# Optimization experiments

Measured on AMD Instinct MI355X. Metric: run time of the kernel, lower is better.

The kernel has to match this reference:

```python
import jax, jax.numpy as jnp
import numpy as np

N, IN_DIM, H, L, NH, LAT = 4096, 16, 128, 4, 8, 16
HD = H // NH
FF = 2 * H
DR_THR = 0.2
LN_EPS = 1e-5


def _ln(x, s, b):
    m = x.mean(-1, keepdims=True)
    v = ((x - m) ** 2).mean(-1, keepdims=True)
    return (x - m) * jax.lax.rsqrt(v + LN_EPS) * s + b


def compute_dr_mask(x_raw):
    eta = x_raw[:, 1] * (2.62 - (-2.62)) + (-2.62)
    phi = x_raw[:, 2] * (3.1416 - (-3.1416)) + (-3.1416)
    deta = eta[:, None] - eta[None, :]
    dphi = phi[:, None] - phi[None, :]
    dphi = jnp.arctan2(jnp.sin(dphi), jnp.cos(dphi))
    dr = jnp.sqrt(deta ** 2 + dphi ** 2)
    return jnp.where(dr <= DR_THR, 0.0, -jnp.inf).astype(jnp.float32)


def setup_inputs() -> dict:
    key = jax.random.key(0)
    ks = jax.random.split(key, 32)
    g = lambda i, shape, s=0.02: (jax.random.normal(ks[i], shape, dtype=jnp.float32) * s)
    inp = {
        'x_raw': jax.random.uniform(ks[0], (N, IN_DIM), dtype=jnp.float32),
        'batch': jnp.zeros((N,), dtype=jnp.int64) if jax.config.read('jax_enable_x64') else jnp.zeros((N,), dtype=jnp.int32),
        'in_w': g(1, (H, IN_DIM), 0.1), 'in_b': jnp.zeros((H,), jnp.float32),
        'ln1_s': jnp.ones((L, H), jnp.float32), 'ln1_b': jnp.zeros((L, H), jnp.float32),
        'qkv_w': g(2, (L, 3 * H, H)), 'qkv_b': jnp.zeros((L, 3 * H), jnp.float32),
        'ao_w': g(3, (L, H, H)), 'ao_b': jnp.zeros((L, H), jnp.float32),
        'ln2_s': jnp.ones((L, H), jnp.float32), 'ln2_b': jnp.zeros((L, H), jnp.float32),
        'f1_w': g(4, (L, FF, H)), 'f1_b': jnp.zeros((L, FF), jnp.float32),
        'f2_w': g(5, (L, H, FF)), 'f2_b': jnp.zeros((L, H), jnp.float32),
        'lat1_w': g(6, (H, H), 0.08), 'lat1_b': jnp.zeros((H,), jnp.float32),
        'lat2_w': g(7, (LAT, H), 0.08), 'lat2_b': jnp.zeros((LAT,), jnp.float32),
        'b1_w': g(8, (H // 2, H), 0.08), 'b1_b': jnp.zeros((H // 2,), jnp.float32),
        'b2_w': g(9, (1, H // 2), 0.008), 'b2_b': jnp.full((1,), -3.0, jnp.float32),
    }
    return inp


def reference(x_raw, batch, in_w, in_b, ln1_s, ln1_b, qkv_w, qkv_b, ao_w, ao_b,
              ln2_s, ln2_b, f1_w, f1_b, f2_w, f2_b,
              lat1_w, lat1_b, lat2_w, lat2_b, b1_w, b1_b, b2_w, b2_b):
    mask = jax.lax.stop_gradient(compute_dr_mask(x_raw))  # [N, N] additive mask
    x = x_raw @ in_w.T + in_b  # [N, H]
    scale = 1.0 / jnp.sqrt(jnp.float32(HD))
    for l in range(L):  # norm_first TransformerEncoderLayer, eval mode (no dropout)
        h = _ln(x, ln1_s[l], ln1_b[l])
        qkv = h @ qkv_w[l].T + qkv_b[l]
        q, k, v = [t.reshape(N, NH, HD) for t in jnp.split(qkv, 3, axis=-1)]
        scores = jnp.einsum('qhd,khd->hqk', q, k) * scale + mask[None]
        attn = jax.nn.softmax(scores, axis=-1)
        o = jnp.einsum('hqk,khd->qhd', attn, v).reshape(N, H)
        x = x + o @ ao_w[l].T + ao_b[l]
        h2 = _ln(x, ln2_s[l], ln2_b[l])
        x = x + jax.nn.relu(h2 @ f1_w[l].T + f1_b[l]) @ f2_w[l].T + f2_b[l]
    lat = jax.nn.relu(x @ lat1_w.T + lat1_b) @ lat2_w.T + lat2_b  # [N, LAT]
    lat = lat / jnp.maximum(jnp.linalg.norm(lat, axis=-1, keepdims=True), 1e-12)
    beta = jax.nn.sigmoid(jax.nn.relu(x @ b1_w.T + b1_b) @ b2_w.T + b2_b)
    beta = jnp.clip(beta, 1e-6, 1 - 1e-6)  # [N, 1]
    return beta, lat
```

## Files before the change

kernel.cpp:

```cpp
#include <hip/hip_runtime.h>
#include <hip/hip_bf16.h>

typedef unsigned short u16;
typedef short short8_t __attribute__((ext_vector_type(8)));
typedef float floatx4 __attribute__((ext_vector_type(4)));

constexpr int NT = 4096, H = 128, CAP = 64;
constexpr int GRID = 256, BLK = 512, GSTRIDE = GRID * BLK;

constexpr int OFF_QKV  = 0;
constexpr int OFF_AO   = 196608;
constexpr int OFF_F1   = 262144;
constexpr int OFF_F2   = 393216;
constexpr int OFF_LAT1 = 524288;
constexpr int OFF_B1   = 540672;
constexpr int OFF_LAT2 = 548864;
constexpr int W_TOTAL  = 550912;

__device__ __forceinline__ float bfu(u16 u) { return __uint_as_float(((unsigned)u) << 16); }
__device__ __forceinline__ u16 f2bf(float f) {
  unsigned u = __float_as_uint(f);
  u += 0x7fffu + ((u >> 16) & 1u);
  return (u16)(u >> 16);
}
__device__ __forceinline__ void unpack8(uint4 u, float* f) {
  f[0] = __uint_as_float(u.x << 16); f[1] = __uint_as_float(u.x & 0xffff0000u);
  f[2] = __uint_as_float(u.y << 16); f[3] = __uint_as_float(u.y & 0xffff0000u);
  f[4] = __uint_as_float(u.z << 16); f[5] = __uint_as_float(u.z & 0xffff0000u);
  f[6] = __uint_as_float(u.w << 16); f[7] = __uint_as_float(u.w & 0xffff0000u);
}
__device__ __forceinline__ short8_t cvt8(const float* bp) {
  const float4 f0 = *(const float4*)bp, f1 = *(const float4*)(bp + 4);
  short8_t r;
  r[0] = (short)f2bf(f0.x); r[1] = (short)f2bf(f0.y);
  r[2] = (short)f2bf(f0.z); r[3] = (short)f2bf(f0.w);
  r[4] = (short)f2bf(f1.x); r[5] = (short)f2bf(f1.y);
  r[6] = (short)f2bf(f1.z); r[7] = (short)f2bf(f1.w);
  return r;
}

struct Prm {
  const float *xr, *in_w, *in_b, *ln1_s, *ln1_b, *qkv_w, *qkv_b, *ao_w, *ao_b,
              *ln2_s, *ln2_b, *f1_w, *f1_b, *f2_w, *f2_b, *lat1_w, *lat1_b,
              *lat2_w, *lat2_b, *b1_w, *b1_b, *b2_w, *b2_b;
  u16* W; u16* QKV0; u16* QKV1; float* Xg; int* NI; int* NC; float* out;
};

__global__ __launch_bounds__(BLK, 2) void prep_kernel(Prm p) {
  const int t = threadIdx.x, bid = blockIdx.x;
  const int lane = t & 63, w = t >> 6;
  const int lr = lane & 15, quad = lane >> 4;
  const int gtid = bid * BLK + t;
  const int r0 = bid * 16;
  const floatx4 FZ = {0.f, 0.f, 0.f, 0.f};

  __shared__ float Xs[16][132];
  __shared__ union {
    unsigned long long words[8][64];
    struct { u16 A16[16][152]; } g;
    u16 QS[16][384];
  } sm;

  for (int i = 49152 + gtid; i < W_TOTAL; i += GSTRIDE) {
    float v;
    if      (i < OFF_AO)   v = p.qkv_w[i];
    else if (i < OFF_F1)   v = p.ao_w[i - OFF_AO];
    else if (i < OFF_F2)   v = p.f1_w[i - OFF_F1];
    else if (i < OFF_LAT1) v = p.f2_w[i - OFF_F2];
    else if (i < OFF_B1)   v = p.lat1_w[i - OFF_LAT1];
    else if (i < OFF_LAT2) v = p.b1_w[i - OFF_B1];
    else                   v = p.lat2_w[i - OFF_LAT2];
    p.W[i] = f2bf(v);
  }
  for (int i = t; i < 16 * H; i += BLK) {
    const int r = i >> 7, c = i & 127;
    const float* xp = p.xr + (size_t)(r0 + r) * 16;
    const float* wp = p.in_w + c * 16;
    float acc = p.in_b[c];
#pragma unroll
    for (int k = 0; k < 16; ++k) acc += xp[k] * wp[k];
    Xs[r][c] = acc;
    p.Xg[(size_t)(r0 + r) * H + c] = acc;
  }
  for (int uu = 0; uu < 2; ++uu) {
    const int q0 = r0 + uu * 8;
    double qe[8], qp_[8];
#pragma unroll
    for (int j = 0; j < 8; ++j) {
      qe[j]  = (double)p.xr[(q0 + j) * 16 + 1] * 5.24 - 2.62;
      qp_[j] = (double)p.xr[(q0 + j) * 16 + 2] * 6.2832 - 3.1416;
    }
    for (int c = 0; c < 8; ++c) {
      const int k = c * 512 + t;
      const double ke = (double)p.xr[k * 16 + 1] * 5.24 - 2.62;
      const double kp = (double)p.xr[k * 16 + 2] * 6.2832 - 3.1416;
#pragma unroll
      for (int j = 0; j < 8; ++j) {
        const double de = qe[j] - ke;
        double dp = qp_[j] - kp;
        dp -= 6.283185307179586 * rint(dp * 0.15915494309189535);
        const unsigned long long bm = __ballot((de * de + dp * dp) <= 0.04);
        if (lane == 0) sm.words[j][c * 8 + w] = bm;
      }
    }
    __syncthreads();
    {
      unsigned long long m = sm.words[w][lane];
      const int cnt = __popcll(m);
      int incl = cnt;
#pragma unroll
      for (int off = 1; off < 64; off <<= 1) {
        const int n = __shfl_up(incl, off);
        if (lane >= off) incl += n;
      }
      int pos = incl - cnt;
      const int qq = q0 + w;
      const int kbase = (lane >> 3) * 512 + (lane & 7) * 64;
      while (m) {
        const int b = __builtin_ctzll(m);
        m &= m - 1;
        if (pos < CAP) p.NI[qq * CAP + pos] = kbase + b;
        ++pos;
      }
      if (lane == 63) p.NC[qq] = incl > CAP ? CAP : incl;
    }
    __syncthreads();
  }
  {
    const int r = t >> 5, j0 = (t & 31) * 4;
    const float4 xv = *(const float4*)&Xs[r][j0];
    float v0 = xv.x, v1 = xv.y, v2 = xv.z, v3 = xv.w;
    float s = v0 + v1 + v2 + v3;
    float ss = v0 * v0 + v1 * v1 + v2 * v2 + v3 * v3;
#pragma unroll
    for (int off = 1; off <= 16; off <<= 1) {
      s += __shfl_xor(s, off); ss += __shfl_xor(ss, off);
    }
    const float mean = s * (1.f / 128.f);
    const float rstd = rsqrtf(ss * (1.f / 128.f) - mean * mean + 1e-5f);
    v0 = (v0 - mean) * rstd * p.ln1_s[j0]     + p.ln1_b[j0];
    v1 = (v1 - mean) * rstd * p.ln1_s[j0 + 1] + p.ln1_b[j0 + 1];
    v2 = (v2 - mean) * rstd * p.ln1_s[j0 + 2] + p.ln1_b[j0 + 2];
    v3 = (v3 - mean) * rstd * p.ln1_s[j0 + 3] + p.ln1_b[j0 + 3];
    uint2 pk;
    pk.x = (unsigned)f2bf(v0) | ((unsigned)f2bf(v1) << 16);
    pk.y = (unsigned)f2bf(v2) | ((unsigned)f2bf(v3) << 16);
    *(uint2*)&sm.g.A16[r][j0] = pk;
  }
  __syncthreads();
  {
    const int c0 = w * 48;
    floatx4 a0 = FZ, a1 = FZ, a2 = FZ;
#pragma unroll
    for (int k0 = 0; k0 < 128; k0 += 32) {
      short8_t a  = *(const short8_t*)&sm.g.A16[lr][k0 + quad * 8];
      short8_t b0 = cvt8(&p.qkv_w[(size_t)(c0 + lr) * 128 + k0 + quad * 8]);
      short8_t b1 = cvt8(&p.qkv_w[(size_t)(c0 + 16 + lr) * 128 + k0 + quad * 8]);
      short8_t b2 = cvt8(&p.qkv_w[(size_t)(c0 + 32 + lr) * 128 + k0 + quad * 8]);
      a0 = __builtin_amdgcn_mfma_f32_16x16x32_bf16(a, b0, a0, 0, 0, 0);
      a1 = __builtin_amdgcn_mfma_f32_16x16x32_bf16(a, b1, a1, 0, 0, 0);
      a2 = __builtin_amdgcn_mfma_f32_16x16x32_bf16(a, b2, a2, 0, 0, 0);
    }
    __syncthreads();
#pragma unroll
    for (int r = 0; r < 4; ++r) {
      const int row = quad * 4 + r;
      sm.QS[row][c0 + lr]      = f2bf(a0[r] + p.qkv_b[c0 + lr]);
      sm.QS[row][c0 + 16 + lr] = f2bf(a1[r] + p.qkv_b[c0 + 16 + lr]);
      sm.QS[row][c0 + 32 + lr] = f2bf(a2[r] + p.qkv_b[c0 + 32 + lr]);
    }
    __syncthreads();
    unsigned long long* d64 = (unsigned long long*)(p.QKV0 + (size_t)r0 * 384);
    const unsigned long long* s64 = (const unsigned long long*)&sm.QS[0][0];
    for (int j = t; j < 1536; j += BLK) d64[j] = s64[j];
  }
}

__global__ __launch_bounds__(BLK, 2) void layer_kernel(Prm p, int l,
                                                       const u16* __restrict__ qsrc,
                                                       u16* __restrict__ qdst) {
  const int t = threadIdx.x, bid = blockIdx.x;
  const int lane = t & 63, w = t >> 6;
  const int lr = lane & 15, quad = lane >> 4;
  const int r0 = bid * 16;
  const floatx4 FZ = {0.f, 0.f, 0.f, 0.f};

  __shared__ float Xs[16][132];
  __shared__ int NIs[16][CAP];
  __shared__ int NCs[16];
  __shared__ union {
    struct { u16 A16[16][152]; u16 FF1[16][280]; } g;
    u16 QS[16][384];
  } sm;

  {
    const int r = t >> 5, j0 = (t & 31) * 4;
    *(float4*)&Xs[r][j0] = *(const float4*)&p.Xg[(size_t)(r0 + r) * H + j0];
    for (int j = t; j < 16 * CAP; j += BLK) (&NIs[0][0])[j] = p.NI[r0 * CAP + j];
    if (t < 16) NCs[t] = p.NC[r0 + t];
  }

  auto stage_x = [&](const float* sc, const float* bi, bool do_ln) {
    const int r = t >> 5, j0 = (t & 31) * 4;
    const float4 xv = *(const float4*)&Xs[r][j0];
    float v0 = xv.x, v1 = xv.y, v2 = xv.z, v3 = xv.w;
    if (do_ln) {
      float s = v0 + v1 + v2 + v3;
      float ss = v0 * v0 + v1 * v1 + v2 * v2 + v3 * v3;
#pragma unroll
      for (int off = 1; off <= 16; off <<= 1) {
        s += __shfl_xor(s, off); ss += __shfl_xor(ss, off);
      }
      const float mean = s * (1.f / 128.f);
      const float rstd = rsqrtf(ss * (1.f / 128.f) - mean * mean + 1e-5f);
      v0 = (v0 - mean) * rstd * sc[j0]     + bi[j0];
      v1 = (v1 - mean) * rstd * sc[j0 + 1] + bi[j0 + 1];
      v2 = (v2 - mean) * rstd * sc[j0 + 2] + bi[j0 + 2];
      v3 = (v3 - mean) * rstd * sc[j0 + 3] + bi[j0 + 3];
    }
    uint2 pk;
    pk.x = (unsigned)f2bf(v0) | ((unsigned)f2bf(v1) << 16);
    pk.y = (unsigned)f2bf(v2) | ((unsigned)f2bf(v3) << 16);
    *(uint2*)&sm.g.A16[r][j0] = pk;
  };
  __syncthreads();

  {
    const int pr = t >> 2, sub = t & 3;
    const int lq = pr >> 3, h = pr & 7;
    const u16* qp = qsrc + (size_t)(r0 + lq) * 384 + h * 16;
    float qv[16];
    { uint4 a = *(const uint4*)qp, b = *(const uint4*)(qp + 8);
      unpack8(a, qv); unpack8(b, qv + 8); }
#pragma unroll
    for (int d = 0; d < 16; ++d) qv[d] *= 0.25f;
    float o[16];
#pragma unroll
    for (int d = 0; d < 16; ++d) o[d] = 0.f;
    float se = 0.f;
    const int cnt = NCs[lq];
    for (int i = sub; i < cnt; i += 4) {
      const int nb = NIs[lq][i];
      const u16* kp = qsrc + (size_t)nb * 384 + 128 + h * 16;
      float kv[16], vv[16];
      { uint4 a = *(const uint4*)kp;         uint4 b = *(const uint4*)(kp + 8);
        unpack8(a, kv); unpack8(b, kv + 8); }
      { uint4 a = *(const uint4*)(kp + 128); uint4 b = *(const uint4*)(kp + 136);
        unpack8(a, vv); unpack8(b, vv + 8); }
      float s0 = 0.f, s1 = 0.f, s2 = 0.f, s3 = 0.f;
#pragma unroll
      for (int d = 0; d < 16; d += 4) {
        s0 += qv[d] * kv[d];         s1 += qv[d + 1] * kv[d + 1];
        s2 += qv[d + 2] * kv[d + 2]; s3 += qv[d + 3] * kv[d + 3];
      }
      const float e = expf((s0 + s1) + (s2 + s3));
      se += e;
#pragma unroll
      for (int d = 0; d < 16; ++d) o[d] += e * vv[d];
    }
#pragma unroll
    for (int d = 0; d < 16; ++d) o[d] += __shfl_xor(o[d], 1);
    se += __shfl_xor(se, 1);
#pragma unroll
    for (int d = 0; d < 16; ++d) o[d] += __shfl_xor(o[d], 2);
    se += __shfl_xor(se, 2);
    if (sub == 0) {
      const float inv = 1.f / se;
      uint4 w0, w1;
      w0.x = (unsigned)f2bf(o[0] * inv)  | ((unsigned)f2bf(o[1] * inv) << 16);
      w0.y = (unsigned)f2bf(o[2] * inv)  | ((unsigned)f2bf(o[3] * inv) << 16);
      w0.z = (unsigned)f2bf(o[4] * inv)  | ((unsigned)f2bf(o[5] * inv) << 16);
      w0.w = (unsigned)f2bf(o[6] * inv)  | ((unsigned)f2bf(o[7] * inv) << 16);
      w1.x = (unsigned)f2bf(o[8] * inv)  | ((unsigned)f2bf(o[9] * inv) << 16);
      w1.y = (unsigned)f2bf(o[10] * inv) | ((unsigned)f2bf(o[11] * inv) << 16);
      w1.z = (unsigned)f2bf(o[12] * inv) | ((unsigned)f2bf(o[13] * inv) << 16);
      w1.w = (unsigned)f2bf(o[14] * inv) | ((unsigned)f2bf(o[15] * inv) << 16);
      *(uint4*)&sm.g.A16[lq][h * 16]     = w0;
      *(uint4*)&sm.g.A16[lq][h * 16 + 8] = w1;
    }
  }
  __syncthreads();
  {
    const u16* Bw = p.W + OFF_AO + l * 16384;
    const float* ab = p.ao_b + l * 128;
    const int col = w * 16 + lr;
    floatx4 acc = FZ;
#pragma unroll
    for (int k0 = 0; k0 < 128; k0 += 32) {
      short8_t a = *(const short8_t*)&sm.g.A16[lr][k0 + quad * 8];
      short8_t b = *(const short8_t*)&Bw[(size_t)col * 128 + k0 + quad * 8];
      acc = __builtin_amdgcn_mfma_f32_16x16x32_bf16(a, b, acc, 0, 0, 0);
    }
    const float bv = ab[col];
#pragma unroll
    for (int r = 0; r < 4; ++r)
      Xs[quad * 4 + r][col] += acc[r] + bv;
  }
  __syncthreads();
  stage_x(p.ln2_s + l * 128, p.ln2_b + l * 128, true);
  __syncthreads();
  {
    const u16* Bw = p.W + OFF_F1 + l * 32768;
    const float* fb = p.f1_b + l * 256;
    const int c0 = w * 32;
    floatx4 a0 = FZ, a1 = FZ;
#pragma unroll
    for (int k0 = 0; k0 < 128; k0 += 32) {
      short8_t a  = *(const short8_t*)&sm.g.A16[lr][k0 + quad * 8];
      short8_t b0 = *(const short8_t*)&Bw[(size_t)(c0 + lr) * 128 + k0 + quad * 8];
      short8_t b1 = *(const short8_t*)&Bw[(size_t)(c0 + 16 + lr) * 128 + k0 + quad * 8];
      a0 = __builtin_amdgcn_mfma_f32_16x16x32_bf16(a, b0, a0, 0, 0, 0);
      a1 = __builtin_amdgcn_mfma_f32_16x16x32_bf16(a, b1, a1, 0, 0, 0);
    }
#pragma unroll
    for (int r = 0; r < 4; ++r) {
      const int row = quad * 4 + r;
      sm.g.FF1[row][c0 + lr]      = f2bf(fmaxf(a0[r] + fb[c0 + lr], 0.f));
      sm.g.FF1[row][c0 + 16 + lr] = f2bf(fmaxf(a1[r] + fb[c0 + 16 + lr], 0.f));
    }
  }
  __syncthreads();
  {
    const u16* Bw = p.W + OFF_F2 + l * 32768;
    const float* fb = p.f2_b + l * 128;
    const int col = w * 16 + lr;
    floatx4 acc = FZ;
#pragma unroll
    for (int k0 = 0; k0 < 256; k0 += 32) {
      short8_t a = *(const short8_t*)&sm.g.FF1[lr][k0 + quad * 8];
      short8_t b = *(const short8_t*)&Bw[(size_t)col * 256 + k0 + quad * 8];
      acc = __builtin_amdgcn_mfma_f32_16x16x32_bf16(a, b, acc, 0, 0, 0);
    }
    const float bv = fb[col];
#pragma unroll
    for (int r = 0; r < 4; ++r)
      Xs[quad * 4 + r][col] += acc[r] + bv;
  }
  __syncthreads();
  if (l < 3) {
    {
      const int r = t >> 5, j0 = (t & 31) * 4;
      *(float4*)&p.Xg[(size_t)(r0 + r) * H + j0] = *(const float4*)&Xs[r][j0];
    }
    stage_x(p.ln1_s + (l + 1) * 128, p.ln1_b + (l + 1) * 128, true);
    __syncthreads();
    {
      const u16* Bw = p.W + OFF_QKV + (l + 1) * 49152;
      const float* qb = p.qkv_b + (l + 1) * 384;
      const int c0 = w * 48;
      floatx4 a0 = FZ, a1 = FZ, a2 = FZ;
#pragma unroll
      for (int k0 = 0; k0 < 128; k0 += 32) {
        short8_t a  = *(const short8_t*)&sm.g.A16[lr][k0 + quad * 8];
        short8_t b0 = *(const short8_t*)&Bw[(size_t)(c0 + lr) * 128 + k0 + quad * 8];
        short8_t b1 = *(const short8_t*)&Bw[(size_t)(c0 + 16 + lr) * 128 + k0 + quad * 8];
        short8_t b2 = *(const short8_t*)&Bw[(size_t)(c0 + 32 + lr) * 128 + k0 + quad * 8];
        a0 = __builtin_amdgcn_mfma_f32_16x16x32_bf16(a, b0, a0, 0, 0, 0);
        a1 = __builtin_amdgcn_mfma_f32_16x16x32_bf16(a, b1, a1, 0, 0, 0);
        a2 = __builtin_amdgcn_mfma_f32_16x16x32_bf16(a, b2, a2, 0, 0, 0);
      }
      __syncthreads();
#pragma unroll
      for (int r = 0; r < 4; ++r) {
        const int row = quad * 4 + r;
        sm.QS[row][c0 + lr]      = f2bf(a0[r] + qb[c0 + lr]);
        sm.QS[row][c0 + 16 + lr] = f2bf(a1[r] + qb[c0 + 16 + lr]);
        sm.QS[row][c0 + 32 + lr] = f2bf(a2[r] + qb[c0 + 32 + lr]);
      }
      __syncthreads();
      unsigned long long* d64 = (unsigned long long*)(qdst + (size_t)r0 * 384);
      const unsigned long long* s64 = (const unsigned long long*)&sm.QS[0][0];
      for (int j = t; j < 1536; j += BLK) d64[j] = s64[j];
    }
  } else {
    stage_x(nullptr, nullptr, false);
    __syncthreads();
    {
      const int c0 = w * 32;
      if (c0 < 192) {
        const u16* Bw = p.W + OFF_LAT1;
        floatx4 a0 = FZ, a1 = FZ;
#pragma unroll
        for (int k0 = 0; k0 < 128; k0 += 32) {
          short8_t a  = *(const short8_t*)&sm.g.A16[lr][k0 + quad * 8];
          short8_t b0 = *(const short8_t*)&Bw[(size_t)(c0 + lr) * 128 + k0 + quad * 8];
          short8_t b1 = *(const short8_t*)&Bw[(size_t)(c0 + 16 + lr) * 128 + k0 + quad * 8];
          a0 = __builtin_amdgcn_mfma_f32_16x16x32_bf16(a, b0, a0, 0, 0, 0);
          a1 = __builtin_amdgcn_mfma_f32_16x16x32_bf16(a, b1, a1, 0, 0, 0);
        }
        const int cA = c0 + lr, cB = c0 + 16 + lr;
        const float bA = cA < 128 ? p.lat1_b[cA] : p.b1_b[cA - 128];
        const float bB = cB < 128 ? p.lat1_b[cB] : p.b1_b[cB - 128];
#pragma unroll
        for (int r = 0; r < 4; ++r) {
          const int row = quad * 4 + r;
          sm.g.FF1[row][cA] = f2bf(fmaxf(a0[r] + bA, 0.f));
          sm.g.FF1[row][cB] = f2bf(fmaxf(a1[r] + bB, 0.f));
        }
      }
    }
    __syncthreads();
    if (t < 256) {
      const int r = t >> 4, c = t & 15;
      float acc = p.lat2_b[c];
      const u16* gw = p.W + OFF_LAT2 + c * 128;
      for (int k = 0; k < 128; ++k) acc += bfu(sm.g.FF1[r][k]) * bfu(gw[k]);
      float ss = acc * acc;
      ss += __shfl_xor(ss, 1); ss += __shfl_xor(ss, 2);
      ss += __shfl_xor(ss, 4); ss += __shfl_xor(ss, 8);
      p.out[NT + (size_t)(r0 + r) * 16 + c] = acc / fmaxf(sqrtf(ss), 1e-12f);
      float v = 0.f;
#pragma unroll
      for (int i = 0; i < 4; ++i)
        v += bfu(sm.g.FF1[r][128 + c * 4 + i]) * p.b2_w[c * 4 + i];
      v += __shfl_xor(v, 1); v += __shfl_xor(v, 2);
      v += __shfl_xor(v, 4); v += __shfl_xor(v, 8);
      if (c == 0) {
        v += p.b2_b[0];
        const float beta = 1.f / (1.f + expf(-v));
        p.out[r0 + r] = fminf(fmaxf(beta, 1e-6f), 1.f - 1e-6f);
      }
    }
  }
}

extern "C" void kernel_launch(void* const* d_in, const int* in_sizes, int n_in,
                              void* d_out, int out_size, void* d_ws, size_t ws_size,
                              hipStream_t stream) {
  Prm prm;
  prm.xr    = (const float*)d_in[0];
  prm.in_w  = (const float*)d_in[2];  prm.in_b  = (const float*)d_in[3];
  prm.ln1_s = (const float*)d_in[4];  prm.ln1_b = (const float*)d_in[5];
  prm.qkv_w = (const float*)d_in[6];  prm.qkv_b = (const float*)d_in[7];
  prm.ao_w  = (const float*)d_in[8];  prm.ao_b  = (const float*)d_in[9];
  prm.ln2_s = (const float*)d_in[10]; prm.ln2_b = (const float*)d_in[11];
  prm.f1_w  = (const float*)d_in[12]; prm.f1_b  = (const float*)d_in[13];
  prm.f2_w  = (const float*)d_in[14]; prm.f2_b  = (const float*)d_in[15];
  prm.lat1_w= (const float*)d_in[16]; prm.lat1_b= (const float*)d_in[17];
  prm.lat2_w= (const float*)d_in[18]; prm.lat2_b= (const float*)d_in[19];
  prm.b1_w  = (const float*)d_in[20]; prm.b1_b  = (const float*)d_in[21];
  prm.b2_w  = (const float*)d_in[22]; prm.b2_b  = (const float*)d_in[23];
  prm.out   = (float*)d_out;

  char* pw = (char*)d_ws;
  prm.W    = (u16*)pw;   pw += ((size_t)W_TOTAL * 2 + 255) & ~(size_t)255;
  prm.QKV0 = (u16*)pw;   pw += (size_t)NT * 384 * 2;
  prm.QKV1 = (u16*)pw;   pw += (size_t)NT * 384 * 2;
  prm.Xg   = (float*)pw; pw += (size_t)NT * H * 4;
  prm.NI   = (int*)pw;   pw += (size_t)NT * CAP * 4;
  prm.NC   = (int*)pw;   pw += (size_t)NT * 4;

  prep_kernel<<<GRID, BLK, 0, stream>>>(prm);
  layer_kernel<<<GRID, BLK, 0, stream>>>(prm, 0, prm.QKV0, prm.QKV1);
  layer_kernel<<<GRID, BLK, 0, stream>>>(prm, 1, prm.QKV1, prm.QKV0);
  layer_kernel<<<GRID, BLK, 0, stream>>>(prm, 2, prm.QKV0, prm.QKV1);
  layer_kernel<<<GRID, BLK, 0, stream>>>(prm, 3, prm.QKV1, nullptr);
}
```

Baseline: 198.1 us.

## Fuse prep and per-layer kernels into one cooperative persistent kernel

Replaces the five kernel launches (prep plus four layer kernels) with a single cooperative kernel that uses grid.sync() between layers. Each block keeps its residual rows, neighbour indices and counts in shared memory for the whole run, so the global Xg/NI/NC round trips go away. It also swaps expf for __expf in the attention softmax and the sigmoid. This saves launch gaps and global traffic, but grid-wide barriers have their own cost and need all 256 blocks to be co-resident.

```diff
diff --git a/kernel.cpp b/kernel.cpp
--- a/kernel.cpp
+++ b/kernel.cpp
@@ -1,5 +1,8 @@
 #include <hip/hip_runtime.h>
 #include <hip/hip_bf16.h>
+#include <hip/hip_cooperative_groups.h>
+
+namespace cg = cooperative_groups;
 
 typedef unsigned short u16;
 typedef short short8_t __attribute__((ext_vector_type(8)));
@@ -43,10 +46,11 @@
   const float *xr, *in_w, *in_b, *ln1_s, *ln1_b, *qkv_w, *qkv_b, *ao_w, *ao_b,
               *ln2_s, *ln2_b, *f1_w, *f1_b, *f2_w, *f2_b, *lat1_w, *lat1_b,
               *lat2_w, *lat2_b, *b1_w, *b1_b, *b2_w, *b2_b;
-  u16* W; u16* QKV0; u16* QKV1; float* Xg; int* NI; int* NC; float* out;
+  u16* W; u16* QKV0; u16* QKV1; float* out;
 };
 
-__global__ __launch_bounds__(BLK, 2) void prep_kernel(Prm p) {
+__global__ __launch_bounds__(BLK, 2) void fused_kernel(Prm p) {
+  cg::grid_group grid = cg::this_grid();
   const int t = threadIdx.x, bid = blockIdx.x;
   const int lane = t & 63, w = t >> 6;
   const int lr = lane & 15, quad = lane >> 4;
@@ -55,11 +59,37 @@
   const floatx4 FZ = {0.f, 0.f, 0.f, 0.f};
 
   __shared__ float Xs[16][132];
+  __shared__ int NIs[16][CAP];
+  __shared__ int NCs[16];
   __shared__ union {
     unsigned long long words[8][64];
-    struct { u16 A16[16][152]; } g;
+    struct { u16 A16[16][152]; u16 FF1[16][280]; } g;
     u16 QS[16][384];
   } sm;
+
+  auto stage_x = [&](const float* sc, const float* bi, bool do_ln) {
+    const int r = t >> 5, j0 = (t & 31) * 4;
+    const float4 xv = *(const float4*)&Xs[r][j0];
+    float v0 = xv.x, v1 = xv.y, v2 = xv.z, v3 = xv.w;
+    if (do_ln) {
+      float s = v0 + v1 + v2 + v3;
+      float ss = v0 * v0 + v1 * v1 + v2 * v2 + v3 * v3;
+#pragma unroll
+      for (int off = 1; off <= 16; off <<= 1) {
+        s += __shfl_xor(s, off); ss += __shfl_xor(ss, off);
+      }
+      const float mean = s * (1.f / 128.f);
+      const float rstd = rsqrtf(ss * (1.f / 128.f) - mean * mean + 1e-5f);
+      v0 = (v0 - mean) * rstd * sc[j0]     + bi[j0];
+      v1 = (v1 - mean) * rstd * sc[j0 + 1] + bi[j0 + 1];
+      v2 = (v2 - mean) * rstd * sc[j0 + 2] + bi[j0 + 2];
+      v3 = (v3 - mean) * rstd * sc[j0 + 3] + bi[j0 + 3];
+    }
+    uint2 pk;
+    pk.x = (unsigned)f2bf(v0) | ((unsigned)f2bf(v1) << 16);
+    pk.y = (unsigned)f2bf(v2) | ((unsigned)f2bf(v3) << 16);
+    *(uint2*)&sm.g.A16[r][j0] = pk;
+  };
 
   for (int i = 49152 + gtid; i < W_TOTAL; i += GSTRIDE) {
     float v;
@@ -80,7 +110,6 @@
 #pragma unroll
     for (int k = 0; k < 16; ++k) acc += xp[k] * wp[k];
     Xs[r][c] = acc;
-    p.Xg[(size_t)(r0 + r) * H + c] = acc;
   }
   for (int uu = 0; uu < 2; ++uu) {
     const int q0 = r0 + uu * 8;
@@ -114,39 +143,19 @@
         if (lane >= off) incl += n;
       }
       int pos = incl - cnt;
-      const int qq = q0 + w;
+      const int lq = uu * 8 + w;
       const int kbase = (lane >> 3) * 512 + (lane & 7) * 64;
       while (m) {
         const int b = __builtin_ctzll(m);
         m &= m - 1;
-        if (pos < CAP) p.NI[qq * CAP + pos] = kbase + b;
+        if (pos < CAP) NIs[lq][pos] = kbase + b;
         ++pos;
       }
-      if (lane == 63) p.NC[qq] = incl > CAP ? CAP : incl;
+      if (lane == 63) NCs[lq] = incl > CAP ? CAP : incl;
     }
     __syncthreads();
   }
-  {
-    const int r = t >> 5, j0 = (t & 31) * 4;
-    const float4 xv = *(const float4*)&Xs[r][j0];
-    float v0 = xv.x, v1 = xv.y, v2 = xv.z, v3 = xv.w;
-    float s = v0 + v1 + v2 + v3;
-    float ss = v0 * v0 + v1 * v1 + v2 * v2 + v3 * v3;
-#pragma unroll
-    for (int off = 1; off <= 16; off <<= 1) {
-      s += __shfl_xor(s, off); ss += __shfl_xor(ss, off);
-    }
-    const float mean = s * (1.f / 128.f);
-    const float rstd = rsqrtf(ss * (1.f / 128.f) - mean * mean + 1e-5f);
-    v0 = (v0 - mean) * rstd * p.ln1_s[j0]     + p.ln1_b[j0];
-    v1 = (v1 - mean) * rstd * p.ln1_s[j0 + 1] + p.ln1_b[j0 + 1];
-    v2 = (v2 - mean) * rstd * p.ln1_s[j0 + 2] + p.ln1_b[j0 + 2];
-    v3 = (v3 - mean) * rstd * p.ln1_s[j0 + 3] + p.ln1_b[j0 + 3];
-    uint2 pk;
-    pk.x = (unsigned)f2bf(v0) | ((unsigned)f2bf(v1) << 16);
-    pk.y = (unsigned)f2bf(v2) | ((unsigned)f2bf(v3) << 16);
-    *(uint2*)&sm.g.A16[r][j0] = pk;
-  }
+  stage_x(p.ln1_s, p.ln1_b, true);
   __syncthreads();
   {
     const int c0 = w * 48;
@@ -174,251 +183,204 @@
     const unsigned long long* s64 = (const unsigned long long*)&sm.QS[0][0];
     for (int j = t; j < 1536; j += BLK) d64[j] = s64[j];
   }
-}
-
-__global__ __launch_bounds__(BLK, 2) void layer_kernel(Prm p, int l,
-                                                       const u16* __restrict__ qsrc,
-                                                       u16* __restrict__ qdst) {
-  const int t = threadIdx.x, bid = blockIdx.x;
-  const int lane = t & 63, w = t >> 6;
-  const int lr = lane & 15, quad = lane >> 4;
-  const int r0 = bid * 16;
-  const floatx4 FZ = {0.f, 0.f, 0.f, 0.f};
-
-  __shared__ float Xs[16][132];
-  __shared__ int NIs[16][CAP];
-  __shared__ int NCs[16];
-  __shared__ union {
-    struct { u16 A16[16][152]; u16 FF1[16][280]; } g;
-    u16 QS[16][384];
-  } sm;
-
-  {
-    const int r = t >> 5, j0 = (t & 31) * 4;
-    *(float4*)&Xs[r][j0] = *(const float4*)&p.Xg[(size_t)(r0 + r) * H + j0];
-    for (int j = t; j < 16 * CAP; j += BLK) (&NIs[0][0])[j] = p.NI[r0 * CAP + j];
-    if (t < 16) NCs[t] = p.NC[r0 + t];
-  }
-
-  auto stage_x = [&](const float* sc, const float* bi, bool do_ln) {
-    const int r = t >> 5, j0 = (t & 31) * 4;
-    const float4 xv = *(const float4*)&Xs[r][j0];
-    float v0 = xv.x, v1 = xv.y, v2 = xv.z, v3 = xv.w;
-    if (do_ln) {
-      float s = v0 + v1 + v2 + v3;
-      float ss = v0 * v0 + v1 * v1 + v2 * v2 + v3 * v3;
-#pragma unroll
-      for (int off = 1; off <= 16; off <<= 1) {
-        s += __shfl_xor(s, off); ss += __shfl_xor(ss, off);
-      }
-      const float mean = s * (1.f / 128.f);
-      const float rstd = rsqrtf(ss * (1.f / 128.f) - mean * mean + 1e-5f);
-      v0 = (v0 - mean) * rstd * sc[j0]     + bi[j0];
-      v1 = (v1 - mean) * rstd * sc[j0 + 1] + bi[j0 + 1];
-      v2 = (v2 - mean) * rstd * sc[j0 + 2] + bi[j0 + 2];
-      v3 = (v3 - mean) * rstd * sc[j0 + 3] + bi[j0 + 3];
-    }
-    uint2 pk;
-    pk.x = (unsigned)f2bf(v0) | ((unsigned)f2bf(v1) << 16);
-    pk.y = (unsigned)f2bf(v2) | ((unsigned)f2bf(v3) << 16);
-    *(uint2*)&sm.g.A16[r][j0] = pk;
-  };
-  __syncthreads();
-
-  {
-    const int pr = t >> 2, sub = t & 3;
-    const int lq = pr >> 3, h = pr & 7;
-    const u16* qp = qsrc + (size_t)(r0 + lq) * 384 + h * 16;
-    float qv[16];
-    { uint4 a = *(const uint4*)qp, b = *(const uint4*)(qp + 8);
-      unpack8(a, qv); unpack8(b, qv + 8); }
-#pragma unroll
-    for (int d = 0; d < 16; ++d) qv[d] *= 0.25f;
-    float o[16];
-#pragma unroll
-    for (int d = 0; d < 16; ++d) o[d] = 0.f;
-    float se = 0.f;
-    const int cnt = NCs[lq];
-    for (int i = sub; i < cnt; i += 4) {
-      const int nb = NIs[lq][i];
-      const u16* kp = qsrc + (size_t)nb * 384 + 128 + h * 16;
-      float kv[16], vv[16];
-      { uint4 a = *(const uint4*)kp;         uint4 b = *(const uint4*)(kp + 8);
-        unpack8(a, kv); unpack8(b, kv + 8); }
-      { uint4 a = *(const uint4*)(kp + 128); uint4 b = *(const uint4*)(kp + 136);
-        unpack8(a, vv); unpack8(b, vv + 8); }
-      float s0 = 0.f, s1 = 0.f, s2 = 0.f, s3 = 0.f;
-#pragma unroll
-      for (int d = 0; d < 16; d += 4) {
-        s0 += qv[d] * kv[d];         s1 += qv[d + 1] * kv[d + 1];
-        s2 += qv[d + 2] * kv[d + 2]; s3 += qv[d + 3] * kv[d + 3];
-      }
-      const float e = expf((s0 + s1) + (s2 + s3));
-      se += e;
-#pragma unroll
-      for (int d = 0; d < 16; ++d) o[d] += e * vv[d];
-    }
-#pragma unroll
-    for (int d = 0; d < 16; ++d) o[d] += __shfl_xor(o[d], 1);
-    se += __shfl_xor(se, 1);
-#pragma unroll
-    for (int d = 0; d < 16; ++d) o[d] += __shfl_xor(o[d], 2);
-    se += __shfl_xor(se, 2);
-    if (sub == 0) {
-      const float inv = 1.f / se;
-      uint4 w0, w1;
-      w0.x = (unsigned)f2bf(o[0] * inv)  | ((unsigned)f2bf(o[1] * inv) << 16);
-      w0.y = (unsigned)f2bf(o[2] * inv)  | ((unsigned)f2bf(o[3] * inv) << 16);
-      w0.z = (unsigned)f2bf(o[4] * inv)  | ((unsigned)f2bf(o[5] * inv) << 16);
-      w0.w = (unsigned)f2bf(o[6] * inv)  | ((unsigned)f2bf(o[7] * inv) << 16);
-      w1.x = (unsigned)f2bf(o[8] * inv)  | ((unsigned)f2bf(o[9] * inv) << 16);
-      w1.y = (unsigned)f2bf(o[10] * inv) | ((unsigned)f2bf(o[11] * inv) << 16);
-      w1.z = (unsigned)f2bf(o[12] * inv) | ((unsigned)f2bf(o[13] * inv) << 16);
-      w1.w = (unsigned)f2bf(o[14] * inv) | ((unsigned)f2bf(o[15] * inv) << 16);
-      *(uint4*)&sm.g.A16[lq][h * 16]     = w0;
-      *(uint4*)&sm.g.A16[lq][h * 16 + 8] = w1;
-    }
-  }
-  __syncthreads();
-  {
-    const u16* Bw = p.W + OFF_AO + l * 16384;
-    const float* ab = p.ao_b + l * 128;
-    const int col = w * 16 + lr;
-    floatx4 acc = FZ;
-#pragma unroll
-    for (int k0 = 0; k0 < 128; k0 += 32) {
-      short8_t a = *(const short8_t*)&sm.g.A16[lr][k0 + quad * 8];
-      short8_t b = *(const short8_t*)&Bw[(size_t)col * 128 + k0 + quad * 8];
-      acc = __builtin_amdgcn_mfma_f32_16x16x32_bf16(a, b, acc, 0, 0, 0);
-    }
-    const float bv = ab[col];
-#pragma unroll
-    for (int r = 0; r < 4; ++r)
-      Xs[quad * 4 + r][col] += acc[r] + bv;
-  }
-  __syncthreads();
-  stage_x(p.ln2_s + l * 128, p.ln2_b + l * 128, true);
-  __syncthreads();
-  {
-    const u16* Bw = p.W + OFF_F1 + l * 32768;
-    const float* fb = p.f1_b + l * 256;
-    const int c0 = w * 32;
-    floatx4 a0 = FZ, a1 = FZ;
-#pragma unroll
-    for (int k0 = 0; k0 < 128; k0 += 32) {
-      short8_t a  = *(const short8_t*)&sm.g.A16[lr][k0 + quad * 8];
-      short8_t b0 = *(const short8_t*)&Bw[(size_t)(c0 + lr) * 128 + k0 + quad * 8];
-      short8_t b1 = *(const short8_t*)&Bw[(size_t)(c0 + 16 + lr) * 128 + k0 + quad * 8];
-      a0 = __builtin_amdgcn_mfma_f32_16x16x32_bf16(a, b0, a0, 0, 0, 0);
-      a1 = __builtin_amdgcn_mfma_f32_16x16x32_bf16(a, b1, a1, 0, 0, 0);
-    }
-#pragma unroll
-    for (int r = 0; r < 4; ++r) {
-      const int row = quad * 4 + r;
-      sm.g.FF1[row][c0 + lr]      = f2bf(fmaxf(a0[r] + fb[c0 + lr], 0.f));
-      sm.g.FF1[row][c0 + 16 + lr] = f2bf(fmaxf(a1[r] + fb[c0 + 16 + lr], 0.f));
-    }
-  }
-  __syncthreads();
-  {
-    const u16* Bw = p.W + OFF_F2 + l * 32768;
-    const float* fb = p.f2_b + l * 128;
-    const int col = w * 16 + lr;
-    floatx4 acc = FZ;
-#pragma unroll
-    for (int k0 = 0; k0 < 256; k0 += 32) {
-      short8_t a = *(const short8_t*)&sm.g.FF1[lr][k0 + quad * 8];
-      short8_t b = *(const short8_t*)&Bw[(size_t)col * 256 + k0 + quad * 8];
-      acc = __builtin_amdgcn_mfma_f32_16x16x32_bf16(a, b, acc, 0, 0, 0);
-    }
-    const float bv = fb[col];
-#pragma unroll
-    for (int r = 0; r < 4; ++r)
-      Xs[quad * 4 + r][col] += acc[r] + bv;
-  }
-  __syncthreads();
-  if (l < 3) {
+  grid.sync();
+
+  for (int l = 0; l < 4; ++l) {
+    const u16* __restrict__ qsrc = (l & 1) ? p.QKV1 : p.QKV0;
+    u16* __restrict__ qdst = (l & 1) ? p.QKV0 : p.QKV1;
+
     {
-      const int r = t >> 5, j0 = (t & 31) * 4;
-      *(float4*)&p.Xg[(size_t)(r0 + r) * H + j0] = *(const float4*)&Xs[r][j0];
-    }
-    stage_x(p.ln1_s + (l + 1) * 128, p.ln1_b + (l + 1) * 128, true);
+      const int pr = t >> 2, sub = t & 3;
+      const int lq = pr >> 3, h = pr & 7;
+      const u16* qp = qsrc + (size_t)(r0 + lq) * 384 + h * 16;
+      float qv[16];
+      { uint4 a = *(const uint4*)qp, b = *(const uint4*)(qp + 8);
+        unpack8(a, qv); unpack8(b, qv + 8); }
+#pragma unroll
+      for (int d = 0; d < 16; ++d) qv[d] *= 0.25f;
+      float o[16];
+#pragma unroll
+      for (int d = 0; d < 16; ++d) o[d] = 0.f;
+      float se = 0.f;
+      const int cnt = NCs[lq];
+      for (int i = sub; i < cnt; i += 4) {
+        const int nb = NIs[lq][i];
+        const u16* kp = qsrc + (size_t)nb * 384 + 128 + h * 16;
+        float kv[16], vv[16];
+        { uint4 a = *(const uint4*)kp;         uint4 b = *(const uint4*)(kp + 8);
+          unpack8(a, kv); unpack8(b, kv + 8); }
+        { uint4 a = *(const uint4*)(kp + 128); uint4 b = *(const uint4*)(kp + 136);
+          unpack8(a, vv); unpack8(b, vv + 8); }
+        float s0 = 0.f, s1 = 0.f, s2 = 0.f, s3 = 0.f;
+#pragma unroll
+        for (int d = 0; d < 16; d += 4) {
+          s0 += qv[d] * kv[d];         s1 += qv[d + 1] * kv[d + 1];
+          s2 += qv[d + 2] * kv[d + 2]; s3 += qv[d + 3] * kv[d + 3];
+        }
+        const float e = __expf((s0 + s1) + (s2 + s3));
+        se += e;
+#pragma unroll
+        for (int d = 0; d < 16; ++d) o[d] += e * vv[d];
+      }
+#pragma unroll
+      for (int d = 0; d < 16; ++d) o[d] += __shfl_xor(o[d], 1);
+      se += __shfl_xor(se, 1);
+#pragma unroll
+      for (int d = 0; d < 16; ++d) o[d] += __shfl_xor(o[d], 2);
+      se += __shfl_xor(se, 2);
+      if (sub == 0) {
+        const float inv = 1.f / se;
+        uint4 w0, w1;
+        w0.x = (unsigned)f2bf(o[0] * inv)  | ((unsigned)f2bf(o[1] * inv) << 16);
+        w0.y = (unsigned)f2bf(o[2] * inv)  | ((unsigned)f2bf(o[3] * inv) << 16);
+        w0.z = (unsigned)f2bf(o[4] * inv)  | ((unsigned)f2bf(o[5] * inv) << 16);
+        w0.w = (unsigned)f2bf(o[6] * inv)  | ((unsigned)f2bf(o[7] * inv) << 16);
+        w1.x = (unsigned)f2bf(o[8] * inv)  | ((unsigned)f2bf(o[9] * inv) << 16);
+        w1.y = (unsigned)f2bf(o[10] * inv) | ((unsigned)f2bf(o[11] * inv) << 16);
+        w1.z = (unsigned)f2bf(o[12] * inv) | ((unsigned)f2bf(o[13] * inv) << 16);
+        w1.w = (unsigned)f2bf(o[14] * inv) | ((unsigned)f2bf(o[15] * inv) << 16);
+        *(uint4*)&sm.g.A16[lq][h * 16]     = w0;
+        *(uint4*)&sm.g.A16[lq][h * 16 + 8] = w1;
+      }
+    }
     __syncthreads();
     {
-      const u16* Bw = p.W + OFF_QKV + (l + 1) * 49152;
-      const float* qb = p.qkv_b + (l + 1) * 384;
-      const int c0 = w * 48;
-      floatx4 a0 = FZ, a1 = FZ, a2 = FZ;
+      const u16* Bw = p.W + OFF_AO + l * 16384;
+      const float* ab = p.ao_b + l * 128;
+      const int col = w * 16 + lr;
+      floatx4 acc = FZ;
+#pragma unroll
+      for (int k0 = 0; k0 < 128; k0 += 32) {
+        short8_t a = *(const short8_t*)&sm.g.A16[lr][k0 + quad * 8];
+        short8_t b = *(const short8_t*)&Bw[(size_t)col * 128 + k0 + quad * 8];
+        acc = __builtin_amdgcn_mfma_f32_16x16x32_bf16(a, b, acc, 0, 0, 0);
+      }
+      const float bv = ab[col];
+#pragma unroll
+      for (int r = 0; r < 4; ++r)
+        Xs[quad * 4 + r][col] += acc[r] + bv;
+    }
+    __syncthreads();
+    stage_x(p.ln2_s + l * 128, p.ln2_b + l * 128, true);
+    __syncthreads();
+    {
+      const u16* Bw = p.W + OFF_F1 + l * 32768;
+      const float* fb = p.f1_b + l * 256;
+      const int c0 = w * 32;
+      floatx4 a0 = FZ, a1 = FZ;
 #pragma unroll
       for (int k0 = 0; k0 < 128; k0 += 32) {
         short8_t a  = *(const short8_t*)&sm.g.A16[lr][k0 + quad * 8];
         short8_t b0 = *(const short8_t*)&Bw[(size_t)(c0 + lr) * 128 + k0 + quad * 8];
         short8_t b1 = *(const short8_t*)&Bw[(size_t)(c0 + 16 + lr) * 128 + k0 + quad * 8];
-        short8_t b2 = *(const short8_t*)&Bw[(size_t)(c0 + 32 + lr) * 128 + k0 + quad * 8];
         a0 = __builtin_amdgcn_mfma_f32_16x16x32_bf16(a, b0, a0, 0, 0, 0);
         a1 = __builtin_amdgcn_mfma_f32_16x16x32_bf16(a, b1, a1, 0, 0, 0);
-        a2 = __builtin_amdgcn_mfma_f32_16x16x32_bf16(a, b2, a2, 0, 0, 0);
-      }
-      __syncthreads();
+      }
 #pragma unroll
       for (int r = 0; r < 4; ++r) {
         const int row = quad * 4 + r;
-        sm.QS[row][c0 + lr]      = f2bf(a0[r] + qb[c0 + lr]);
-        sm.QS[row][c0 + 16 + lr] = f2bf(a1[r] + qb[c0 + 16 + lr]);
-        sm.QS[row][c0 + 32 + lr] = f2bf(a2[r] + qb[c0 + 32 + lr]);
-      }
+        sm.g.FF1[row][c0 + lr]      = f2bf(fmaxf(a0[r] + fb[c0 + lr], 0.f));
+        sm.g.FF1[row][c0 + 16 + lr] = f2bf(fmaxf(a1[r] + fb[c0 + 16 + lr], 0.f));
+      }
+    }
+    __syncthreads();
+    {
+      const u16* Bw = p.W + OFF_F2 + l * 32768;
+      const float* fb = p.f2_b + l * 128;
+      const int col = w * 16 + lr;
+      floatx4 acc = FZ;
+#pragma unroll
+      for (int k0 = 0; k0 < 256; k0 += 32) {
+        short8_t a = *(const short8_t*)&sm.g.FF1[lr][k0 + quad * 8];
+        short8_t b = *(const short8_t*)&Bw[(size_t)col * 256 + k0 + quad * 8];
+        acc = __builtin_amdgcn_mfma_f32_16x16x32_bf16(a, b, acc, 0, 0, 0);
+      }
+      const float bv = fb[col];
+#pragma unroll
+      for (int r = 0; r < 4; ++r)
+        Xs[quad * 4 + r][col] += acc[r] + bv;
+    }
+    __syncthreads();
+    if (l < 3) {
+      stage_x(p.ln1_s + (l + 1) * 128, p.ln1_b + (l + 1) * 128, true);
       __syncthreads();
-      unsigned long long* d64 = (unsigned long long*)(qdst + (size_t)r0 * 384);
-      const unsigned long long* s64 = (const unsigned long long*)&sm.QS[0][0];
-      for (int j = t; j < 1536; j += BLK) d64[j] = s64[j];
-    }
-  } else {
-    stage_x(nullptr, nullptr, false);
-    __syncthreads();
-    {
-      const int c0 = w * 32;
-      if (c0 < 192) {
-        const u16* Bw = p.W + OFF_LAT1;
-        floatx4 a0 = FZ, a1 = FZ;
+      {
+        const u16* Bw = p.W + OFF_QKV + (l + 1) * 49152;
+        const float* qb = p.qkv_b + (l + 1) * 384;
+        const int c0 = w * 48;
+        floatx4 a0 = FZ, a1 = FZ, a2 = FZ;
 #pragma unroll
         for (int k0 = 0; k0 < 128; k0 += 32) {
           short8_t a  = *(const short8_t*)&sm.g.A16[lr][k0 + quad * 8];
           short8_t b0 = *(const short8_t*)&Bw[(size_t)(c0 + lr) * 128 + k0 + quad * 8];
           short8_t b1 = *(const short8_t*)&Bw[(size_t)(c0 + 16 + lr) * 128 + k0 + quad * 8];
+          short8_t b2 = *(const short8_t*)&Bw[(size_t)(c0 + 32 + lr) * 128 + k0 + quad * 8];
           a0 = __builtin_amdgcn_mfma_f32_16x16x32_bf16(a, b0, a0, 0, 0, 0);
           a1 = __builtin_amdgcn_mfma_f32_16x16x32_bf16(a, b1, a1, 0, 0, 0);
+          a2 = __builtin_amdgcn_mfma_f32_16x16x32_bf16(a, b2, a2, 0, 0, 0);
         }
-        const int cA = c0 + lr, cB = c0 + 16 + lr;
-        const float bA = cA < 128 ? p.lat1_b[cA] : p.b1_b[cA - 128];
-        const float bB = cB < 128 ? p.lat1_b[cB] : p.b1_b[cB - 128];
+        __syncthreads();
 #pragma unroll
         for (int r = 0; r < 4; ++r) {
           const int row = quad * 4 + r;
-          sm.g.FF1[row][cA] = f2bf(fmaxf(a0[r] + bA, 0.f));
-          sm.g.FF1[row][cB] = f2bf(fmaxf(a1[r] + bB, 0.f));
+          sm.QS[row][c0 + lr]      = f2bf(a0[r] + qb[c0 + lr]);
+          sm.QS[row][c0 + 16 + lr] = f2bf(a1[r] + qb[c0 + 16 + lr]);
+          sm.QS[row][c0 + 32 + lr] = f2bf(a2[r] + qb[c0 + 32 + lr]);
         }
-      }
-    }
-    __syncthreads();
-    if (t < 256) {
-      const int r = t >> 4, c = t & 15;
-      float acc = p.lat2_b[c];
-      const u16* gw = p.W + OFF_LAT2 + c * 128;
-      for (int k = 0; k < 128; ++k) acc += bfu(sm.g.FF1[r][k]) * bfu(gw[k]);
-      float ss = acc * acc;
-      ss += __shfl_xor(ss, 1); ss += __shfl_xor(ss, 2);
-      ss += __shfl_xor(ss, 4); ss += __shfl_xor(ss, 8);
-      p.out[NT + (size_t)(r0 + r) * 16 + c] = acc / fmaxf(sqrtf(ss), 1e-12f);
-      float v = 0.f;
-#pragma unroll
-      for (int i = 0; i < 4; ++i)
-        v += bfu(sm.g.FF1[r][128 + c * 4 + i]) * p.b2_w[c * 4 + i];
-      v += __shfl_xor(v, 1); v += __shfl_xor(v, 2);
-      v += __shfl_xor(v, 4); v += __shfl_xor(v, 8);
-      if (c == 0) {
-        v += p.b2_b[0];
-        const float beta = 1.f / (1.f + expf(-v));
-        p.out[r0 + r] = fminf(fmaxf(beta, 1e-6f), 1.f - 1e-6f);
+        __syncthreads();
+        unsigned long long* d64 = (unsigned long long*)(qdst + (size_t)r0 * 384);
+        const unsigned long long* s64 = (const unsigned long long*)&sm.QS[0][0];
+        for (int j = t; j < 1536; j += BLK) d64[j] = s64[j];
+      }
+      grid.sync();
+    } else {
+      stage_x(nullptr, nullptr, false);
+      __syncthreads();
+      {
+        const int c0 = w * 32;
+        if (c0 < 192) {
+          const u16* Bw = p.W + OFF_LAT1;
+          floatx4 a0 = FZ, a1 = FZ;
+#pragma unroll
+          for (int k0 = 0; k0 < 128; k0 += 32) {
+            short8_t a  = *(const short8_t*)&sm.g.A16[lr][k0 + quad * 8];
+            short8_t b0 = *(const short8_t*)&Bw[(size_t)(c0 + lr) * 128 + k0 + quad * 8];
+            short8_t b1 = *(const short8_t*)&Bw[(size_t)(c0 + 16 + lr) * 128 + k0 + quad * 8];
+            a0 = __builtin_amdgcn_mfma_f32_16x16x32_bf16(a, b0, a0, 0, 0, 0);
+            a1 = __builtin_amdgcn_mfma_f32_16x16x32_bf16(a, b1, a1, 0, 0, 0);
+          }
+          const int cA = c0 + lr, cB = c0 + 16 + lr;
+          const float bA = cA < 128 ? p.lat1_b[cA] : p.b1_b[cA - 128];
+          const float bB = cB < 128 ? p.lat1_b[cB] : p.b1_b[cB - 128];
+#pragma unroll
+          for (int r = 0; r < 4; ++r) {
+            const int row = quad * 4 + r;
+            sm.g.FF1[row][cA] = f2bf(fmaxf(a0[r] + bA, 0.f));
+            sm.g.FF1[row][cB] = f2bf(fmaxf(a1[r] + bB, 0.f));
+          }
+        }
+      }
+      __syncthreads();
+      if (t < 256) {
+        const int r = t >> 4, c = t & 15;
+        float acc = p.lat2_b[c];
+        const u16* gw = p.W + OFF_LAT2 + c * 128;
+        for (int k = 0; k < 128; ++k) acc += bfu(sm.g.FF1[r][k]) * bfu(gw[k]);
+        float ss = acc * acc;
+        ss += __shfl_xor(ss, 1); ss += __shfl_xor(ss, 2);
+        ss += __shfl_xor(ss, 4); ss += __shfl_xor(ss, 8);
+        p.out[NT + (size_t)(r0 + r) * 16 + c] = acc / fmaxf(sqrtf(ss), 1e-12f);
+        float v = 0.f;
+#pragma unroll
+        for (int i = 0; i < 4; ++i)
+          v += bfu(sm.g.FF1[r][128 + c * 4 + i]) * p.b2_w[c * 4 + i];
+        v += __shfl_xor(v, 1); v += __shfl_xor(v, 2);
+        v += __shfl_xor(v, 4); v += __shfl_xor(v, 8);
+        if (c == 0) {
+          v += p.b2_b[0];
+          const float beta = 1.f / (1.f + __expf(-v));
+          p.out[r0 + r] = fminf(fmaxf(beta, 1e-6f), 1.f - 1e-6f);
+        }
       }
     }
   }
@@ -446,13 +408,8 @@
   prm.W    = (u16*)pw;   pw += ((size_t)W_TOTAL * 2 + 255) & ~(size_t)255;
   prm.QKV0 = (u16*)pw;   pw += (size_t)NT * 384 * 2;
   prm.QKV1 = (u16*)pw;   pw += (size_t)NT * 384 * 2;
-  prm.Xg   = (float*)pw; pw += (size_t)NT * H * 4;
-  prm.NI   = (int*)pw;   pw += (size_t)NT * CAP * 4;
-  prm.NC   = (int*)pw;   pw += (size_t)NT * 4;
-
-  prep_kernel<<<GRID, BLK, 0, stream>>>(prm);
-  layer_kernel<<<GRID, BLK, 0, stream>>>(prm, 0, prm.QKV0, prm.QKV1);
-  layer_kernel<<<GRID, BLK, 0, stream>>>(prm, 1, prm.QKV1, prm.QKV0);
-  layer_kernel<<<GRID, BLK, 0, stream>>>(prm, 2, prm.QKV0, prm.QKV1);
-  layer_kernel<<<GRID, BLK, 0, stream>>>(prm, 3, prm.QKV1, nullptr);
+
+  void* args[] = {&prm};
+  hipLaunchCooperativeKernel((void*)fused_kernel, dim3(GRID), dim3(BLK),
+                             args, 0, stream);
 }
```

Result: slower. 346.9 us (+75.1%).
